# Kernel tuning notes

Measured on AMD Instinct MI355X. Metric: run time of the kernel, lower is better.

The kernel has to match this reference:

```python
import jax, jax.numpy as jnp
import numpy as np
import math

B, L, H, D, S, R = 2, 1024, 8, 64, 10, 128


def setup_inputs() -> dict:
    key = jax.random.key(0)
    k1, k2, k3, k4, k5, k6 = jax.random.split(key, 6)
    return {
        "queries": jax.random.normal(k1, (B, L, H, D), jnp.float32),
        "keys": jax.random.normal(k2, (B, L, H, D), jnp.float32),
        "freqs": jax.random.normal(k3, (H, D, S), jnp.float32),
        "offsets": jax.random.normal(k4, (H, D, S), jnp.float32),
        "gains": jax.random.normal(k5, (H, D, S), jnp.float32),
        "z": jax.random.normal(k6, (B, H, D, 2 * S, R), jnp.float32),
    }


def reference(queries, keys, freqs, offsets, gains, z):
    length = queries.shape[1]
    idx = jnp.arange(length, dtype=queries.dtype)  # [L]
    fr = jax.nn.sigmoid(freqs) / 2.0  # [H,D,S]
    two_pi = 2.0 * math.pi
    # phases: [H,D,L,S]
    phases_q = two_pi * fr[:, :, None, :] * idx[None, None, :, None] + offsets[:, :, None, :]
    phases_k = two_pi * fr[:, :, None, :] * idx[None, None, :, None]
    # interleave cos/sin along last dim -> [H,D,L,2S]
    omega_q = jnp.stack([jnp.cos(phases_q), jnp.sin(phases_q)], axis=-1).reshape(
        phases_q.shape[0], phases_q.shape[1], length, 2 * phases_q.shape[-1])
    omega_k = jnp.stack([jnp.cos(phases_k), jnp.sin(phases_k)], axis=-1).reshape(
        phases_k.shape[0], phases_k.shape[1], length, 2 * phases_k.shape[-1])
    # gains: softplus then repeat(1,1,2) -> concat copies along last dim [H,D,2S]
    g = jax.nn.softplus(gains)
    g2 = jnp.concatenate([g, g], axis=-1)
    scale = 1.0 / math.sqrt(z.shape[-1] * queries.shape[-1])  # 1/sqrt(R*D)
    zs = z * (g2[None, :, :, :, None] * scale)  # [B,H,D,2S,R]
    # fused: qbar[b,h,d,l,r] = sum_s omega_q[h,d,l,s] * zs[b,h,d,s,r];
    # qhat[b,l,h,r] = sum_d qbar[b,l,h,d,r] * queries[b,l,h,d]
    qhat = jnp.einsum('hdls,bhdsr,blhd->blhr', omega_q, zs, queries)
    khat = jnp.einsum('hdls,bhdsr,blhd->blhr', omega_k, zs, keys)
    return (qhat, khat)
```

## Files before the change

kernel.cpp:

```cpp
#include <hip/hip_runtime.h>
#include <math.h>


typedef short bf16x8 __attribute__((ext_vector_type(8)));
typedef float f32x16 __attribute__((ext_vector_type(16)));

__device__ __forceinline__ unsigned int rnd_bf16(float x) {
    union { float f; unsigned int u; } v; v.f = x;
    return v.u + 0x8000u;
}
__device__ __forceinline__ unsigned int pack_bf16(float c, float s) {
    return __builtin_amdgcn_perm(rnd_bf16(s), rnd_bf16(c), 0x07060302u);
}

__global__ __launch_bounds__(256) void prep_tab(
    const float* __restrict__ freqs, const float* __restrict__ offsets,
    const float* __restrict__ gains, float2* __restrict__ frof,
    float* __restrict__ gs)
{
    int i = blockIdx.x * 256 + threadIdx.x;
    int hd = i / 20, tt = i - hd * 20;
    int jm = (tt < 10) ? tt : tt - 10;
    float gn = gains[hd * 10 + jm];
    float g = fmaxf(gn, 0.0f) + log1pf(__expf(-fabsf(gn)));
    gs[i] = g * 0.011048543456039806f;
    if (i < 5120) {
        int hh = i / 640, rem = i - hh * 640;
        int ss = rem >> 6, dd = rem & 63;
        int src = (hh * 64 + dd) * 10 + ss;
        float fr = 0.5f / (1.0f + __expf(-freqs[src]));
        frof[i] = make_float2(fr, offsets[src] * 0.15915494309189535f);
        frof[5120 + i] = make_float2(fr, 0.0f);
    }
}

__global__ __launch_bounds__(256) void prep_z(
    const float* __restrict__ z, const float* __restrict__ gs,
    uint4* __restrict__ zt)
{
    int bid = blockIdx.x;
    int bh = bid / 20, kb = bid - bh * 20;
    int h = bh & 7;
    int dh = (kb >= 10) ? 1 : 0, s = kb - dh * 10;
    int t = threadIdx.x;
    const float* zb = z + (size_t)bh * 163840;
    const float* gsb = gs + h * 1280;
    uint4* outb = zt + (size_t)bid * 1024;

    #pragma unroll
    for (int i = 0; i < 4; i++) {
        int e = i * 256 + t;
        int r = (e >> 1) & 127, c8 = e & 1;
        int dl0 = i * 8 + c8 * 4;
        unsigned int u[4];
        #pragma unroll
        for (int m = 0; m < 4; m++) {
            int d = dh * 32 + dl0 + m;
            float ve = zb[((size_t)d * 20 + 2 * s) * 128 + r] * gsb[d * 20 + 2 * s];
            float vo = zb[((size_t)d * 20 + 2 * s + 1) * 128 + r] * gsb[d * 20 + 2 * s + 1];
            u[m] = pack_bf16(ve, vo);
        }
        outb[e] = make_uint4(u[0], u[1], u[2], u[3]);
    }
}

__global__ __launch_bounds__(256, 4) void spe_gemm(
    const float* __restrict__ queries, const float* __restrict__ keys,
    const float2* __restrict__ frof, const unsigned short* __restrict__ zt,
    float* __restrict__ out)
{
    __shared__ unsigned int At[2][1024];

    int bid = blockIdx.x;
    int h = bid & 7;
    int u = bid >> 3;
    int qk = u & 1, b = (u >> 1) & 1, lt = u >> 2;
    int l0 = lt * 32;

    int t = threadIdx.x, w = t >> 6, lane = t & 63;
    int ml = lane & 31, hi = lane >> 5;
    int arow = t >> 3, pg = t & 7;

    const float* qsrc = (qk ? keys : queries)
                      + ((size_t)(b * 1024 + l0 + arow) * 8 + h) * 64 + pg * 4;
    const float2* fob = frof + qk * 5120 + h * 640 + pg * 4;
    const unsigned short* bbase = zt + (size_t)(b * 8 + h) * 163840
                                + (w * 32 + ml) * 16 + hi * 8;
    float lf = (float)(l0 + arow);
    unsigned int awz = arow * 32 + ((pg ^ (arow & 7)) << 2);

    float4 qf = *(const float4*)(qsrc);

    {
        const float4* fp = (const float4*)(fob);
        float4 fA = fp[0], fB = fp[1];
        float p0 = __builtin_amdgcn_fractf(fmaf(fA.x, lf, fA.y));
        float p1 = __builtin_amdgcn_fractf(fmaf(fA.z, lf, fA.w));
        float p2 = __builtin_amdgcn_fractf(fmaf(fB.x, lf, fB.y));
        float p3 = __builtin_amdgcn_fractf(fmaf(fB.z, lf, fB.w));
        uint4 a4;
        a4.x = pack_bf16(__builtin_amdgcn_cosf(p0) * qf.x, __builtin_amdgcn_sinf(p0) * qf.x);
        a4.y = pack_bf16(__builtin_amdgcn_cosf(p1) * qf.y, __builtin_amdgcn_sinf(p1) * qf.y);
        a4.z = pack_bf16(__builtin_amdgcn_cosf(p2) * qf.z, __builtin_amdgcn_sinf(p2) * qf.z);
        a4.w = pack_bf16(__builtin_amdgcn_cosf(p3) * qf.w, __builtin_amdgcn_sinf(p3) * qf.w);
        *(uint4*)&At[0][awz] = a4;
    }

    f32x16 acc = {};

    #pragma unroll 2
    for (int kb = 0; kb < 20; kb++) {
        __syncthreads();
        int cur = kb & 1;

        const unsigned short* tp = bbase + (size_t)kb * 8192;
        bf16x8 b0 = *(const bf16x8*)(tp);
        bf16x8 b1 = *(const bf16x8*)(tp + 2048);
        bf16x8 b2 = *(const bf16x8*)(tp + 4096);
        bf16x8 b3 = *(const bf16x8*)(tp + 6144);

        if (kb < 19) {
            int kn = kb + 1;
            int dh = (kn >= 10) ? 1 : 0;
            int s = kn - dh * 10;
            if (kn == 10) qf = *(const float4*)(qsrc + 32);
            const float4* fp = (const float4*)(fob + s * 64 + dh * 32);
            float4 fA = fp[0], fB = fp[1];
            float p0 = __builtin_amdgcn_fractf(fmaf(fA.x, lf, fA.y));
            float p1 = __builtin_amdgcn_fractf(fmaf(fA.z, lf, fA.w));
            float p2 = __builtin_amdgcn_fractf(fmaf(fB.x, lf, fB.y));
            float p3 = __builtin_amdgcn_fractf(fmaf(fB.z, lf, fB.w));
            uint4 a4;
            a4.x = pack_bf16(__builtin_amdgcn_cosf(p0) * qf.x, __builtin_amdgcn_sinf(p0) * qf.x);
            a4.y = pack_bf16(__builtin_amdgcn_cosf(p1) * qf.y, __builtin_amdgcn_sinf(p1) * qf.y);
            a4.z = pack_bf16(__builtin_amdgcn_cosf(p2) * qf.z, __builtin_amdgcn_sinf(p2) * qf.z);
            a4.w = pack_bf16(__builtin_amdgcn_cosf(p3) * qf.w, __builtin_amdgcn_sinf(p3) * qf.w);
            *(uint4*)&At[cur ^ 1][awz] = a4;
        }

        #pragma unroll
        for (int ks = 0; ks < 4; ks++) {
            bf16x8 a = *(const bf16x8*)&At[cur][ml * 32 + (((ks * 2 + hi) ^ (ml & 7)) << 2)];
            bf16x8 bb = (ks == 0) ? b0 : (ks == 1) ? b1 : (ks == 2) ? b2 : b3;
            acc = __builtin_amdgcn_mfma_f32_32x32x16_bf16(a, bb, acc, 0, 0, 0);
        }
    }

    float* ob = out + (size_t)qk * 2097152 + (size_t)b * 1048576
              + (size_t)h * 128 + w * 32 + ml;
    #pragma unroll
    for (int reg = 0; reg < 16; reg++) {
        int row = l0 + (reg & 3) + 8 * (reg >> 2) + 4 * hi;
        ob[(size_t)row * 1024] = acc[reg];
    }
}

extern "C" void kernel_launch(void* const* d_in, const int* in_sizes, int n_in,
                              void* d_out, int out_size, void* d_ws, size_t ws_size,
                              hipStream_t stream) {
    const float* queries = (const float*)d_in[0];
    const float* keys    = (const float*)d_in[1];
    const float* freqs   = (const float*)d_in[2];
    const float* offsets = (const float*)d_in[3];
    const float* gains   = (const float*)d_in[4];
    const float* z       = (const float*)d_in[5];
    float* out = (float*)d_out;

    float2* frof = (float2*)d_ws;
    float* gs = (float*)((char*)d_ws + 81920);
    uint4* zt = (uint4*)((char*)d_ws + 122880);

    prep_tab<<<40, 256, 0, stream>>>(freqs, offsets, gains, frof, gs);
    prep_z<<<320, 256, 0, stream>>>(z, gs, zt);
    spe_gemm<<<1024, 256, 0, stream>>>(queries, keys, frof,
                                       (const unsigned short*)zt, out);
}
```

Measured before the change: 104.1 us.

## Fuse table prep into z prep kernel and prefetch B fragments one step ahead

Merges the prep_tab kernel into prep_z: each block computes its slice of the frequency/offset table and the softplus gain scales for its own rows into shared memory, removing one launch and the global gs buffer. In the GEMM kernel, the z tile fragments for the next k-step are loaded a full iteration ahead into registers, so global load latency overlaps the current MFMAs. This costs extra registers for the double-buffered B fragments, and the last iteration does a redundant reload and sin/cos recompute.

```diff
diff --git a/kernel.cpp b/kernel.cpp
--- a/kernel.cpp
+++ b/kernel.cpp
@@ -13,18 +13,22 @@
     return __builtin_amdgcn_perm(rnd_bf16(s), rnd_bf16(c), 0x07060302u);
 }
 
-__global__ __launch_bounds__(256) void prep_tab(
+__global__ __launch_bounds__(256) void prep_z(
     const float* __restrict__ freqs, const float* __restrict__ offsets,
-    const float* __restrict__ gains, float2* __restrict__ frof,
-    float* __restrict__ gs)
+    const float* __restrict__ gains, const float* __restrict__ z,
+    uint4* __restrict__ zt, float2* __restrict__ frof)
 {
-    int i = blockIdx.x * 256 + threadIdx.x;
-    int hd = i / 20, tt = i - hd * 20;
-    int jm = (tt < 10) ? tt : tt - 10;
-    float gn = gains[hd * 10 + jm];
-    float g = fmaxf(gn, 0.0f) + log1pf(__expf(-fabsf(gn)));
-    gs[i] = g * 0.011048543456039806f;
-    if (i < 5120) {
+    const float scale = 0.011048543456039806f;
+    int bid = blockIdx.x;
+    int bh = bid / 20, kb = bid - bh * 20;
+    int h = bh & 7;
+    int dh = (kb >= 10) ? 1 : 0, s = kb - dh * 10;
+    int t = threadIdx.x;
+
+    __shared__ float gsl[64];
+
+    if (t < 16) {
+        int i = bid * 16 + t;
         int hh = i / 640, rem = i - hh * 640;
         int ss = rem >> 6, dd = rem & 63;
         int src = (hh * 64 + dd) * 10 + ss;
@@ -32,19 +36,16 @@
         frof[i] = make_float2(fr, offsets[src] * 0.15915494309189535f);
         frof[5120 + i] = make_float2(fr, 0.0f);
     }
-}
+    if (t < 64) {
+        int dl = t >> 1, par = t & 1;
+        int tt = 2 * s + par;
+        int jm = (tt < 10) ? tt : tt - 10;
+        float gn = gains[(h * 64 + dh * 32 + dl) * 10 + jm];
+        gsl[t] = (fmaxf(gn, 0.0f) + log1pf(__expf(-fabsf(gn)))) * scale;
+    }
+    __syncthreads();
 
-__global__ __launch_bounds__(256) void prep_z(
-    const float* __restrict__ z, const float* __restrict__ gs,
-    uint4* __restrict__ zt)
-{
-    int bid = blockIdx.x;
-    int bh = bid / 20, kb = bid - bh * 20;
-    int h = bh & 7;
-    int dh = (kb >= 10) ? 1 : 0, s = kb - dh * 10;
-    int t = threadIdx.x;
     const float* zb = z + (size_t)bh * 163840;
-    const float* gsb = gs + h * 1280;
     uint4* outb = zt + (size_t)bid * 1024;
 
     #pragma unroll
@@ -55,9 +56,10 @@
         unsigned int u[4];
         #pragma unroll
         for (int m = 0; m < 4; m++) {
-            int d = dh * 32 + dl0 + m;
-            float ve = zb[((size_t)d * 20 + 2 * s) * 128 + r] * gsb[d * 20 + 2 * s];
-            float vo = zb[((size_t)d * 20 + 2 * s + 1) * 128 + r] * gsb[d * 20 + 2 * s + 1];
+            int dl = dl0 + m;
+            int d = dh * 32 + dl;
+            float ve = zb[((size_t)d * 20 + 2 * s) * 128 + r] * gsl[dl * 2];
+            float vo = zb[((size_t)d * 20 + 2 * s + 1) * 128 + r] * gsl[dl * 2 + 1];
             u[m] = pack_bf16(ve, vo);
         }
         outb[e] = make_uint4(u[0], u[1], u[2], u[3]);
@@ -91,6 +93,10 @@
 
     float4 qf = *(const float4*)(qsrc);
 
+    bf16x8 n0 = *(const bf16x8*)(bbase);
+    bf16x8 n1 = *(const bf16x8*)(bbase + 2048);
+    bf16x8 n2 = *(const bf16x8*)(bbase + 4096);
+    bf16x8 n3 = *(const bf16x8*)(bbase + 6144);
     {
         const float4* fp = (const float4*)(fob);
         float4 fA = fp[0], fB = fp[1];
@@ -113,14 +119,16 @@
         __syncthreads();
         int cur = kb & 1;
 
-        const unsigned short* tp = bbase + (size_t)kb * 8192;
-        bf16x8 b0 = *(const bf16x8*)(tp);
-        bf16x8 b1 = *(const bf16x8*)(tp + 2048);
-        bf16x8 b2 = *(const bf16x8*)(tp + 4096);
-        bf16x8 b3 = *(const bf16x8*)(tp + 6144);
+        bf16x8 c0 = n0, c1 = n1, c2 = n2, c3 = n3;
 
-        if (kb < 19) {
-            int kn = kb + 1;
+        int kn = (kb < 19) ? kb + 1 : 19;
+        const unsigned short* tp = bbase + (size_t)kn * 8192;
+        n0 = *(const bf16x8*)(tp);
+        n1 = *(const bf16x8*)(tp + 2048);
+        n2 = *(const bf16x8*)(tp + 4096);
+        n3 = *(const bf16x8*)(tp + 6144);
+
+        {
             int dh = (kn >= 10) ? 1 : 0;
             int s = kn - dh * 10;
             if (kn == 10) qf = *(const float4*)(qsrc + 32);
@@ -141,7 +149,7 @@
         #pragma unroll
         for (int ks = 0; ks < 4; ks++) {
             bf16x8 a = *(const bf16x8*)&At[cur][ml * 32 + (((ks * 2 + hi) ^ (ml & 7)) << 2)];
-            bf16x8 bb = (ks == 0) ? b0 : (ks == 1) ? b1 : (ks == 2) ? b2 : b3;
+            bf16x8 bb = (ks == 0) ? c0 : (ks == 1) ? c1 : (ks == 2) ? c2 : c3;
             acc = __builtin_amdgcn_mfma_f32_32x32x16_bf16(a, bb, acc, 0, 0, 0);
         }
     }
@@ -167,11 +175,9 @@
     float* out = (float*)d_out;
 
     float2* frof = (float2*)d_ws;
-    float* gs = (float*)((char*)d_ws + 81920);
-    uint4* zt = (uint4*)((char*)d_ws + 122880);
+    uint4* zt = (uint4*)((char*)d_ws + 81920);
 
-    prep_tab<<<40, 256, 0, stream>>>(freqs, offsets, gains, frof, gs);
-    prep_z<<<320, 256, 0, stream>>>(z, gs, zt);
+    prep_z<<<320, 256, 0, stream>>>(freqs, offsets, gains, z, zt, frof);
     spe_gemm<<<1024, 256, 0, stream>>>(queries, keys, frof,
                                        (const unsigned short*)zt, out);
 }
```

Measured after the change: 101.0 us. 3.1% less time.
